# Performance work log

Measured on AMD Instinct MI355X. Metric: run time of the kernel, lower is better.

Reference implementation:

```python
import jax, jax.numpy as jnp
import numpy as np
import math

D_MODEL = 512
N_HEADS = 8
D_K = D_MODEL // N_HEADS
N_SAMPLES = 16
BETA = 1.0
SCALE = 1.0 / math.sqrt(D_K)
PROPOSAL_TEMP = 0.5


def setup_inputs() -> dict:
    key = jax.random.key(0)
    ks = jax.random.split(key, 9)
    B, S = 2, 512
    x = jax.random.normal(ks[0], (B, S, D_MODEL), dtype=jnp.float32)
    init = lambda k: jax.random.normal(k, (D_MODEL, D_MODEL), dtype=jnp.float32) * 0.02
    return {
        "x": x,
        "Wq": init(ks[1]), "bq": jnp.zeros((D_MODEL,), jnp.float32),
        "Wk": init(ks[2]), "bk": jnp.zeros((D_MODEL,), jnp.float32),
        "Wv": init(ks[3]), "bv": jnp.zeros((D_MODEL,), jnp.float32),
        "Wo": init(ks[4]), "bo": jnp.zeros((D_MODEL,), jnp.float32),
    }


def _importance_sampled_weights(scores):
    # scores: [B,H,S,S]. Replicates the per-row Python loop, fully vectorized.
    B, H, Sq, Sk = scores.shape
    target = jax.nn.softmax(scores * BETA, axis=-1)            # [B,H,Sq,Sk]
    # optimal proposal: 0.5*target + 0.5*uniform
    prop = PROPOSAL_TEMP * target + (1.0 - PROPOSAL_TEMP) / Sk
    R = B * H * Sq
    tf = target.reshape(R, Sk)
    pf = prop.reshape(R, Sk)
    # tsu_backend.sample_binary_layer(log(p/(1-p))) == Bernoulli(p) sampling
    s = jax.random.bernoulli(jax.random.key(42), pf[:, None, :], (R, N_SAMPLES, Sk))
    # importance weight = prod(target[sel]) / (prod(prop[sel]) * prod(1-prop[~sel]))
    pt = jnp.prod(jnp.where(s, tf[:, None, :], 1.0), axis=-1)                 # [R,N]
    pp = jnp.prod(jnp.where(s, pf[:, None, :], 1.0 - pf[:, None, :]), axis=-1)
    valid = (s.sum(-1) > 0) & (pp > 0)
    w = jnp.where(valid, pt / jnp.maximum(pp, 1e-38), 0.0)
    ws = w.sum(-1, keepdims=True)
    w = jnp.where(ws > 0, w / jnp.maximum(ws, 1e-38), 1.0 / N_SAMPLES)        # [R,N]
    wa = jnp.einsum('rn,rnk->rk', w, s.astype(jnp.float32))                   # [R,Sk]
    was = wa.sum(-1, keepdims=True)
    wa = jnp.where(was > 0, wa / jnp.maximum(was, 1e-38), 1.0 / Sk)
    return wa.reshape(B, H, Sq, Sk)


def reference(x, Wq, bq, Wk, bk, Wv, bv, Wo, bo):
    B, S, Dm = x.shape
    proj = lambda W, b: (x @ W + b).reshape(B, S, N_HEADS, D_K).transpose(0, 2, 1, 3)
    Q = proj(Wq, bq)  # [B,H,S,dk]
    K = proj(Wk, bk)
    V = proj(Wv, bv)
    scores = jnp.einsum('bhqd,bhkd->bhqk', Q, K) * SCALE
    # torch builds weights via torch.tensor(...) which detaches => constant w.r.t. params
    attn = jax.lax.stop_gradient(_importance_sampled_weights(scores))
    out = jnp.einsum('bhqk,bhkd->bhqd', attn, V)
    out = out.transpose(0, 2, 1, 3).reshape(B, S, Dm)
    return out @ Wo + bo
```

## Files before the change

### kernel.cpp

```cpp
#include <hip/hip_runtime.h>
#include <cstdint>
#include <cstddef>


#define ROTL(x, r) __builtin_rotateleft32((x), (r))

#define QR8(s)                                                                \
  x0[0]+=x1[0];x0[1]+=x1[1];x0[2]+=x1[2];x0[3]+=x1[3];                        \
  x0[4]+=x1[4];x0[5]+=x1[5];x0[6]+=x1[6];x0[7]+=x1[7];                        \
  x1[0]=ROTL(x1[0],s);x1[1]=ROTL(x1[1],s);x1[2]=ROTL(x1[2],s);                \
  x1[3]=ROTL(x1[3],s);x1[4]=ROTL(x1[4],s);x1[5]=ROTL(x1[5],s);                \
  x1[6]=ROTL(x1[6],s);x1[7]=ROTL(x1[7],s);                                    \
  x1[0]^=x0[0];x1[1]^=x0[1];x1[2]^=x0[2];x1[3]^=x0[3];                        \
  x1[4]^=x0[4];x1[5]^=x0[5];x1[6]^=x0[6];x1[7]^=x0[7];
#define INJ8(X, Y)                                                            \
  x0[0]+=(X);x0[1]+=(X);x0[2]+=(X);x0[3]+=(X);                                \
  x0[4]+=(X);x0[5]+=(X);x0[6]+=(X);x0[7]+=(X);                                \
  x1[0]+=(Y);x1[1]+=(Y);x1[2]+=(Y);x1[3]+=(Y);                                \
  x1[4]+=(Y);x1[5]+=(Y);x1[6]+=(Y);x1[7]+=(Y);
#define INJ8Y(Y)                                                              \
  x1[0]+=(Y);x1[1]+=(Y);x1[2]+=(Y);x1[3]+=(Y);                                \
  x1[4]+=(Y);x1[5]+=(Y);x1[6]+=(Y);x1[7]+=(Y);

__global__ __launch_bounds__(256)
void qkv_gemm(const float* __restrict__ x,
              const float* __restrict__ Wq, const float* __restrict__ bq,
              const float* __restrict__ Wk, const float* __restrict__ bk,
              const float* __restrict__ Wv, const float* __restrict__ bv,
              float* __restrict__ Qw, float* __restrict__ KTw,
              float* __restrict__ Vw) {
  const float* W; const float* bias; float* out;
  if (blockIdx.z == 0)      { W = Wq; bias = bq; out = Qw; }
  else if (blockIdx.z == 1) { W = Wk; bias = bk; out = KTw; }
  else                      { W = Wv; bias = bv; out = Vw; }

  __shared__ float At[32][68];
  __shared__ float Bs[32][64];
  const int tid = threadIdx.x;
  const int tx = tid & 15, ty = tid >> 4;
  const int row0 = blockIdx.x * 64, col0 = blockIdx.y * 64;
  float acc[4][4] = {};

  for (int kk = 0; kk < 512; kk += 32) {
    const int ar = tid >> 2;
#pragma unroll
    for (int i = 0; i < 2; ++i) {
      const int kc = ((tid & 3) << 3) + (i << 2);
      const float4 a4 =
          *(const float4*)&x[(size_t)(row0 + ar) * 512 + kk + kc];
      At[kc + 0][ar] = a4.x; At[kc + 1][ar] = a4.y;
      At[kc + 2][ar] = a4.z; At[kc + 3][ar] = a4.w;
    }
#pragma unroll
    for (int i = 0; i < 2; ++i) {
      const int idx = tid + (i << 8);
      const int br = idx >> 4, bc = (idx & 15) << 2;
      *(float4*)&Bs[br][bc] =
          *(const float4*)&W[(size_t)(kk + br) * 512 + col0 + bc];
    }
    __syncthreads();
#pragma unroll
    for (int p = 0; p < 32; ++p) {
      const float4 a4 = *(const float4*)&At[p][ty << 2];
      const float4 b4 = *(const float4*)&Bs[p][tx << 2];
      acc[0][0] = fmaf(a4.x, b4.x, acc[0][0]); acc[0][1] = fmaf(a4.x, b4.y, acc[0][1]);
      acc[0][2] = fmaf(a4.x, b4.z, acc[0][2]); acc[0][3] = fmaf(a4.x, b4.w, acc[0][3]);
      acc[1][0] = fmaf(a4.y, b4.x, acc[1][0]); acc[1][1] = fmaf(a4.y, b4.y, acc[1][1]);
      acc[1][2] = fmaf(a4.y, b4.z, acc[1][2]); acc[1][3] = fmaf(a4.y, b4.w, acc[1][3]);
      acc[2][0] = fmaf(a4.z, b4.x, acc[2][0]); acc[2][1] = fmaf(a4.z, b4.y, acc[2][1]);
      acc[2][2] = fmaf(a4.z, b4.z, acc[2][2]); acc[2][3] = fmaf(a4.z, b4.w, acc[2][3]);
      acc[3][0] = fmaf(a4.w, b4.x, acc[3][0]); acc[3][1] = fmaf(a4.w, b4.y, acc[3][1]);
      acc[3][2] = fmaf(a4.w, b4.z, acc[3][2]); acc[3][3] = fmaf(a4.w, b4.w, acc[3][3]);
    }
    __syncthreads();
  }
  const bool isK = (blockIdx.z == 1);
#pragma unroll
  for (int i = 0; i < 4; ++i) {
    const int row = row0 + (ty << 2) + i;
    const int b = row >> 9, s = row & 511;
#pragma unroll
    for (int j = 0; j < 4; ++j) {
      const int col = col0 + (tx << 2) + j;
      const int h = col >> 6, d = col & 63;
      const float v = acc[i][j] + bias[col];
      if (isK)
        out[(((size_t)(b * 8 + h) * 64 + d) * 512) + s] = v;
      else
        out[(((size_t)(b * 8 + h) * 512 + s) * 64) + d] = v;
    }
  }
}

__global__ __launch_bounds__(256)
void out_gemm(const float* __restrict__ A, const float* __restrict__ W,
              const float* __restrict__ bias, float* __restrict__ C) {
  __shared__ float At[32][68];
  __shared__ float Bs[32][64];
  const int tid = threadIdx.x;
  const int tx = tid & 15, ty = tid >> 4;
  const int row0 = blockIdx.x * 64, col0 = blockIdx.y * 64;
  float acc[4][4] = {};

  for (int kk = 0; kk < 512; kk += 32) {
    const int ar = tid >> 2;
#pragma unroll
    for (int i = 0; i < 2; ++i) {
      const int kc = ((tid & 3) << 3) + (i << 2);
      const float4 a4 =
          *(const float4*)&A[(size_t)(row0 + ar) * 512 + kk + kc];
      At[kc + 0][ar] = a4.x; At[kc + 1][ar] = a4.y;
      At[kc + 2][ar] = a4.z; At[kc + 3][ar] = a4.w;
    }
#pragma unroll
    for (int i = 0; i < 2; ++i) {
      const int idx = tid + (i << 8);
      const int br = idx >> 4, bc = (idx & 15) << 2;
      *(float4*)&Bs[br][bc] =
          *(const float4*)&W[(size_t)(kk + br) * 512 + col0 + bc];
    }
    __syncthreads();
#pragma unroll
    for (int p = 0; p < 32; ++p) {
      const float4 a4 = *(const float4*)&At[p][ty << 2];
      const float4 b4 = *(const float4*)&Bs[p][tx << 2];
      acc[0][0] = fmaf(a4.x, b4.x, acc[0][0]); acc[0][1] = fmaf(a4.x, b4.y, acc[0][1]);
      acc[0][2] = fmaf(a4.x, b4.z, acc[0][2]); acc[0][3] = fmaf(a4.x, b4.w, acc[0][3]);
      acc[1][0] = fmaf(a4.y, b4.x, acc[1][0]); acc[1][1] = fmaf(a4.y, b4.y, acc[1][1]);
      acc[1][2] = fmaf(a4.y, b4.z, acc[1][2]); acc[1][3] = fmaf(a4.y, b4.w, acc[1][3]);
      acc[2][0] = fmaf(a4.z, b4.x, acc[2][0]); acc[2][1] = fmaf(a4.z, b4.y, acc[2][1]);
      acc[2][2] = fmaf(a4.z, b4.z, acc[2][2]); acc[2][3] = fmaf(a4.z, b4.w, acc[2][3]);
      acc[3][0] = fmaf(a4.w, b4.x, acc[3][0]); acc[3][1] = fmaf(a4.w, b4.y, acc[3][1]);
      acc[3][2] = fmaf(a4.w, b4.z, acc[3][2]); acc[3][3] = fmaf(a4.w, b4.w, acc[3][3]);
    }
    __syncthreads();
  }
#pragma unroll
  for (int i = 0; i < 4; ++i) {
    const int row = row0 + (ty << 2) + i;
#pragma unroll
    for (int j = 0; j < 4; ++j) {
      const int col = col0 + (tx << 2) + j;
      C[(size_t)row * 512 + col] = acc[i][j] + bias[col];
    }
  }
}

__global__ __launch_bounds__(256)
void fused_sample(const float* __restrict__ Q, const float* __restrict__ KT,
                  const float* __restrict__ V, float* __restrict__ ao) {
  const int r = blockIdx.x;
  const int bh = r >> 9, q = r & 511;
  const int b = r >> 12, h = (r >> 9) & 7;
  const int tid = threadIdx.x;
  __shared__ __align__(16) float qs[64];
  __shared__ float red[8];
  __shared__ float tf[512];
  __shared__ __align__(16) uint32_t pscu2[512];
  __shared__ float wa[512];
  __shared__ float wr[16];
  __shared__ float redc[8];
  __shared__ float psum[4][64];
  __shared__ int   list[512];
  __shared__ int   cnt;

  if (tid == 0) cnt = 0;
  if (tid < 64) qs[tid] = Q[((size_t)bh * 512 + q) * 64 + tid];
  __syncthreads();

  float sc[2];
#pragma unroll
  for (int ii = 0; ii < 2; ++ii) {
    const int k = tid + (ii << 8);
    const float* Kp = KT + (size_t)bh * 64 * 512 + k;
    float s = 0.f;
#pragma unroll
    for (int d4 = 0; d4 < 16; ++d4) {
      const float4 qv = ((const float4*)qs)[d4];
      const float k0 = Kp[(size_t)(d4 * 4 + 0) * 512];
      const float k1 = Kp[(size_t)(d4 * 4 + 1) * 512];
      const float k2 = Kp[(size_t)(d4 * 4 + 2) * 512];
      const float k3 = Kp[(size_t)(d4 * 4 + 3) * 512];
      s = fmaf(qv.x, k0, s); s = fmaf(qv.y, k1, s);
      s = fmaf(qv.z, k2, s); s = fmaf(qv.w, k3, s);
    }
    sc[ii] = s * 0.125f;
  }
  float mx = fmaxf(sc[0], sc[1]);
  for (int m = 1; m < 64; m <<= 1) mx = fmaxf(mx, __shfl_xor(mx, m));
  if ((tid & 63) == 0) red[tid >> 6] = mx;
  __syncthreads();
  const float rowmax = fmaxf(fmaxf(red[0], red[1]), fmaxf(red[2], red[3]));
  const float e0 = expf(sc[0] - rowmax);
  const float e1 = expf(sc[1] - rowmax);
  float ssum = e0 + e1;
  for (int m = 1; m < 64; m <<= 1) ssum += __shfl_xor(ssum, m);
  if ((tid & 63) == 0) red[4 + (tid >> 6)] = ssum;
  __syncthreads();
  const float tot = red[4] + red[5] + red[6] + red[7];
  const float t0 = e0 / tot, t1 = e1 / tot;
  tf[tid] = t0; tf[tid + 256] = t1;
  wa[tid] = 0.f; wa[tid + 256] = 0.f;
  {
    const float p0 = fmaf(0.5f, t0, 0.0009765625f);
    const float p1 = fmaf(0.5f, t1, 0.0009765625f);
    {
      const int k = tid;
      pscu2[(((k & 31) >> 2) << 6) + ((k >> 5) << 2) + (k & 3)] =
          ((uint32_t)ceilf(p0 * 8388608.0f)) << 9;
    }
    {
      const int k = tid + 256;
      pscu2[(((k & 31) >> 2) << 6) + ((k >> 5) << 2) + (k & 3)] =
          ((uint32_t)ceilf(p1 * 8388608.0f)) << 9;
    }
    float ql = (1.f - p0) * (1.f - p1);
    for (int m = 1; m < 64; m <<= 1) ql *= __shfl_xor(ql, m);
    if ((tid & 63) == 0) redc[4 + (tid >> 6)] = ql;
  }
  __syncthreads();
  const float Qrow = redc[4] * redc[5] * redc[6] * redc[7];

  const int n = tid >> 4, t = tid & 15;
  const int k0i = t << 5;
  const uint32_t cbase =
      (uint32_t)r * 8192u + (uint32_t)n * 512u + (uint32_t)k0i + 42u;
  uint32_t bits = 0u;
#pragma unroll
  for (int jb = 0; jb < 32; jb += 8) {
    uint32_t x0[8], x1[8];
#pragma unroll
    for (int i = 0; i < 8; ++i) {
      const uint32_t c = cbase + (uint32_t)(jb + i);
      x0[i] = c;
      x1[i] = ROTL(c, 13) ^ c;
    }
    QR8(15) QR8(26) QR8(6)
    INJ8(42u, 0x1BD11BF1u)
    QR8(17) QR8(29) QR8(16) QR8(24)
    INJ8(0x1BD11BF0u, 2u)
    QR8(13) QR8(15) QR8(26) QR8(6)
    INJ8Y(45u)
    QR8(17) QR8(29) QR8(16) QR8(24)
    INJ8(42u, 0x1BD11BF4u)
    QR8(13) QR8(15) QR8(26) QR8(6)
    INJ8(0x1BD11BF0u, 5u)
    const uint4 pA = *(const uint4*)&pscu2[((jb >> 2) << 6) + (t << 2)];
    const uint4 pB = *(const uint4*)&pscu2[(((jb >> 2) + 1) << 6) + (t << 2)];
    bits |= (uint32_t)((x0[0] ^ x1[0]) < pA.x) << (jb + 0);
    bits |= (uint32_t)((x0[1] ^ x1[1]) < pA.y) << (jb + 1);
    bits |= (uint32_t)((x0[2] ^ x1[2]) < pA.z) << (jb + 2);
    bits |= (uint32_t)((x0[3] ^ x1[3]) < pA.w) << (jb + 3);
    bits |= (uint32_t)((x0[4] ^ x1[4]) < pB.x) << (jb + 4);
    bits |= (uint32_t)((x0[5] ^ x1[5]) < pB.y) << (jb + 5);
    bits |= (uint32_t)((x0[6] ^ x1[6]) < pB.z) << (jb + 6);
    bits |= (uint32_t)((x0[7] ^ x1[7]) < pB.w) << (jb + 7);
  }

  float ptl = 1.f, ratl = 1.f;
  int cl = __popc(bits);
  {
    uint32_t bb = bits;
    while (bb) {
      const int j = __builtin_ctz(bb);
      bb &= bb - 1u;
      const float tv = tf[k0i + j];
      const float p = fmaf(0.5f, tv, 0.0009765625f);
      ptl *= tv;
      ratl *= p / (1.f - p);
    }
  }
#pragma unroll
  for (int m = 1; m < 16; m <<= 1) {
    ptl *= __shfl_xor(ptl, m);
    ratl *= __shfl_xor(ratl, m);
    cl += __shfl_xor(cl, m);
  }
  if (t == 0) {
    const float pp = Qrow * ratl;
    wr[n] = (cl > 0 && pp > 0.f) ? (ptl / fmaxf(pp, 1e-38f)) : 0.f;
  }
  __syncthreads();
  float wsum = 0.f;
#pragma unroll
  for (int m2 = 0; m2 < 16; ++m2) wsum += wr[m2];
  const float wn = (wsum > 0.f) ? (wr[n] / fmaxf(wsum, 1e-38f)) : 0.0625f;
  {
    uint32_t bb = bits;
    while (bb) {
      const int j = __builtin_ctz(bb);
      bb &= bb - 1u;
      atomicAdd(&wa[k0i + j], wn);
    }
  }
  __syncthreads();

  float sp = wa[tid] + wa[tid + 256];
  for (int m = 1; m < 64; m <<= 1) sp += __shfl_xor(sp, m);
  if ((tid & 63) == 0) redc[tid >> 6] = sp;
  if (wa[tid] > 0.f)       { const int i = atomicAdd(&cnt, 1); list[i] = tid; }
  if (wa[tid + 256] > 0.f) { const int i = atomicAdd(&cnt, 1); list[i] = tid + 256; }
  __syncthreads();
  const float was = redc[0] + redc[1] + redc[2] + redc[3];
  const int nnz = cnt;

  const int g = tid >> 6, d = tid & 63;
  const float* Vb = V + ((size_t)(b * 8 + h) * 512) * 64;
  float acc = 0.f;
  if (was > 0.f) {
    const float inv = 1.f / fmaxf(was, 1e-38f);
    for (int i = g; i < nnz; i += 4) {
      const int k = list[i];
      acc = fmaf(wa[k] * inv, Vb[(size_t)k * 64 + d], acc);
    }
  } else {
    for (int k = g; k < 512; k += 4) acc += Vb[(size_t)k * 64 + d];
    acc *= 0.001953125f;
  }
  psum[g][d] = acc;
  __syncthreads();
  if (g == 0) {
    ao[((size_t)(b * 512 + q) * 512) + h * 64 + d] =
        psum[0][d] + psum[1][d] + psum[2][d] + psum[3][d];
  }
}

extern "C" void kernel_launch(void* const* d_in, const int* in_sizes, int n_in,
                              void* d_out, int out_size, void* d_ws,
                              size_t ws_size, hipStream_t stream) {
  const float* x  = (const float*)d_in[0];
  const float* Wq = (const float*)d_in[1];
  const float* bq = (const float*)d_in[2];
  const float* Wk = (const float*)d_in[3];
  const float* bk = (const float*)d_in[4];
  const float* Wv = (const float*)d_in[5];
  const float* bv = (const float*)d_in[6];
  const float* Wo = (const float*)d_in[7];
  const float* bo = (const float*)d_in[8];
  float* out = (float*)d_out;

  float* ws = (float*)d_ws;
  float* Qw = ws;
  float* KT = ws + 524288;
  float* Vw = ws + 1048576;
  float* ao = ws + 1572864;

  dim3 gq(16, 8, 3);
  qkv_gemm<<<gq, 256, 0, stream>>>(x, Wq, bq, Wk, bk, Wv, bv, Qw, KT, Vw);
  fused_sample<<<8192, 256, 0, stream>>>(Qw, KT, Vw, ao);
  dim3 go(16, 8);
  out_gemm<<<go, 256, 0, stream>>>(ao, Wo, bo, out);
}
```

Before: 260.8 us.

## Fuse output projection into sampling kernel with atomic accumulation

```diff
diff --git a/kernel.cpp b/kernel.cpp
--- a/kernel.cpp
+++ b/kernel.cpp
@@ -27,8 +27,22 @@
               const float* __restrict__ Wq, const float* __restrict__ bq,
               const float* __restrict__ Wk, const float* __restrict__ bk,
               const float* __restrict__ Wv, const float* __restrict__ bv,
+              const float* __restrict__ bo, float* __restrict__ outp,
               float* __restrict__ Qw, float* __restrict__ KTw,
               float* __restrict__ Vw) {
+  const int tid = threadIdx.x;
+  if (blockIdx.z == 3) {
+    const int blk = blockIdx.y * 16 + blockIdx.x;
+    const size_t base4 = (size_t)blk * 1024 + tid;
+    const float4* bo4 = (const float4*)bo;
+    float4* out4 = (float4*)outp;
+#pragma unroll
+    for (int i = 0; i < 4; ++i) {
+      const size_t idx4 = base4 + (size_t)i * 256;
+      out4[idx4] = bo4[idx4 & 127];
+    }
+    return;
+  }
   const float* W; const float* bias; float* out;
   if (blockIdx.z == 0)      { W = Wq; bias = bq; out = Qw; }
   else if (blockIdx.z == 1) { W = Wk; bias = bk; out = KTw; }
@@ -36,7 +50,6 @@
 
   __shared__ float At[32][68];
   __shared__ float Bs[32][64];
-  const int tid = threadIdx.x;
   const int tx = tid & 15, ty = tid >> 4;
   const int row0 = blockIdx.x * 64, col0 = blockIdx.y * 64;
   float acc[4][4] = {};
@@ -93,62 +106,9 @@
 }
 
 __global__ __launch_bounds__(256)
-void out_gemm(const float* __restrict__ A, const float* __restrict__ W,
-              const float* __restrict__ bias, float* __restrict__ C) {
-  __shared__ float At[32][68];
-  __shared__ float Bs[32][64];
-  const int tid = threadIdx.x;
-  const int tx = tid & 15, ty = tid >> 4;
-  const int row0 = blockIdx.x * 64, col0 = blockIdx.y * 64;
-  float acc[4][4] = {};
-
-  for (int kk = 0; kk < 512; kk += 32) {
-    const int ar = tid >> 2;
-#pragma unroll
-    for (int i = 0; i < 2; ++i) {
-      const int kc = ((tid & 3) << 3) + (i << 2);
-      const float4 a4 =
-          *(const float4*)&A[(size_t)(row0 + ar) * 512 + kk + kc];
-      At[kc + 0][ar] = a4.x; At[kc + 1][ar] = a4.y;
-      At[kc + 2][ar] = a4.z; At[kc + 3][ar] = a4.w;
-    }
-#pragma unroll
-    for (int i = 0; i < 2; ++i) {
-      const int idx = tid + (i << 8);
-      const int br = idx >> 4, bc = (idx & 15) << 2;
-      *(float4*)&Bs[br][bc] =
-          *(const float4*)&W[(size_t)(kk + br) * 512 + col0 + bc];
-    }
-    __syncthreads();
-#pragma unroll
-    for (int p = 0; p < 32; ++p) {
-      const float4 a4 = *(const float4*)&At[p][ty << 2];
-      const float4 b4 = *(const float4*)&Bs[p][tx << 2];
-      acc[0][0] = fmaf(a4.x, b4.x, acc[0][0]); acc[0][1] = fmaf(a4.x, b4.y, acc[0][1]);
-      acc[0][2] = fmaf(a4.x, b4.z, acc[0][2]); acc[0][3] = fmaf(a4.x, b4.w, acc[0][3]);
-      acc[1][0] = fmaf(a4.y, b4.x, acc[1][0]); acc[1][1] = fmaf(a4.y, b4.y, acc[1][1]);
-      acc[1][2] = fmaf(a4.y, b4.z, acc[1][2]); acc[1][3] = fmaf(a4.y, b4.w, acc[1][3]);
-      acc[2][0] = fmaf(a4.z, b4.x, acc[2][0]); acc[2][1] = fmaf(a4.z, b4.y, acc[2][1]);
-      acc[2][2] = fmaf(a4.z, b4.z, acc[2][2]); acc[2][3] = fmaf(a4.z, b4.w, acc[2][3]);
-      acc[3][0] = fmaf(a4.w, b4.x, acc[3][0]); acc[3][1] = fmaf(a4.w, b4.y, acc[3][1]);
-      acc[3][2] = fmaf(a4.w, b4.z, acc[3][2]); acc[3][3] = fmaf(a4.w, b4.w, acc[3][3]);
-    }
-    __syncthreads();
-  }
-#pragma unroll
-  for (int i = 0; i < 4; ++i) {
-    const int row = row0 + (ty << 2) + i;
-#pragma unroll
-    for (int j = 0; j < 4; ++j) {
-      const int col = col0 + (tx << 2) + j;
-      C[(size_t)row * 512 + col] = acc[i][j] + bias[col];
-    }
-  }
-}
-
-__global__ __launch_bounds__(256)
 void fused_sample(const float* __restrict__ Q, const float* __restrict__ KT,
-                  const float* __restrict__ V, float* __restrict__ ao) {
+                  const float* __restrict__ V, const float* __restrict__ Wo,
+                  float* __restrict__ outp) {
   const int r = blockIdx.x;
   const int bh = r >> 9, q = r & 511;
   const int b = r >> 12, h = (r >> 9) & 7;
@@ -161,6 +121,7 @@
   __shared__ float wr[16];
   __shared__ float redc[8];
   __shared__ float psum[4][64];
+  __shared__ float o_s[64];
   __shared__ int   list[512];
   __shared__ int   cnt;
 
@@ -319,9 +280,22 @@
   }
   psum[g][d] = acc;
   __syncthreads();
-  if (g == 0) {
-    ao[((size_t)(b * 512 + q) * 512) + h * 64 + d] =
-        psum[0][d] + psum[1][d] + psum[2][d] + psum[3][d];
+  if (g == 0)
+    o_s[d] = psum[0][d] + psum[1][d] + psum[2][d] + psum[3][d];
+  __syncthreads();
+
+  {
+    const float* Wh = Wo + ((size_t)h * 64) * 512;
+    float a0 = 0.f, a1 = 0.f;
+#pragma unroll 8
+    for (int dd = 0; dd < 64; ++dd) {
+      const float ov = o_s[dd];
+      a0 = fmaf(ov, Wh[(size_t)dd * 512 + tid], a0);
+      a1 = fmaf(ov, Wh[(size_t)dd * 512 + tid + 256], a1);
+    }
+    float* orow = outp + ((size_t)(b * 512 + q)) * 512;
+    atomicAdd(&orow[tid], a0);
+    atomicAdd(&orow[tid + 256], a1);
   }
 }
 
@@ -343,11 +317,9 @@
   float* Qw = ws;
   float* KT = ws + 524288;
   float* Vw = ws + 1048576;
-  float* ao = ws + 1572864;
-
-  dim3 gq(16, 8, 3);
-  qkv_gemm<<<gq, 256, 0, stream>>>(x, Wq, bq, Wk, bk, Wv, bv, Qw, KT, Vw);
-  fused_sample<<<8192, 256, 0, stream>>>(Qw, KT, Vw, ao);
-  dim3 go(16, 8);
-  out_gemm<<<go, 256, 0, stream>>>(ao, Wo, bo, out);
+
+  dim3 gq(16, 8, 4);
+  qkv_gemm<<<gq, 256, 0, stream>>>(x, Wq, bq, Wk, bk, Wv, bv, bo, out,
+                                   Qw, KT, Vw);
+  fused_sample<<<8192, 256, 0, stream>>>(Qw, KT, Vw, Wo, out);
 }
```

New measurement: 254.3 us. -2.5%, faster.
